# Kernel tuning notes

Hardware: AMD Instinct MI355X
Metric: run time of the kernel (lower is better)

Reference implementation:

```python
import jax, jax.numpy as jnp
import numpy as np

B, N, D, E = 128, 512, 256, 8192  # graphs, nodes/graph, embed_dim, edges/graph
K = int(np.ceil(0.8 * N))         # TopKPooling ratio=0.8 -> k per graph


def setup_inputs() -> dict:
    key = jax.random.key(0)
    ks = jax.random.split(key, 16)
    Ntot = B * N
    x = jax.random.normal(ks[0], (Ntot, 4), jnp.float32)
    offs = (jnp.arange(B, dtype=jnp.int32) * N)[:, None]
    src = (jax.random.randint(ks[1], (B, E), 0, N, jnp.int32) + offs).reshape(-1)
    dst = (jax.random.randint(ks[2], (B, E), 0, N, jnp.int32) + offs).reshape(-1)
    s = 0.05
    w = lambda k, shape: jax.random.normal(k, shape, jnp.float32) * s
    return {
        'x': x, 'src': src, 'dst': dst,
        'Wr1': w(ks[3], (4, D)), 'Ws1': w(ks[4], (4, D)), 'b1': jnp.zeros((D,), jnp.float32),
        'Wr2': w(ks[5], (D, D)), 'Ws2': w(ks[6], (D, D)), 'b2': jnp.zeros((D,), jnp.float32),
        'Wr3': w(ks[7], (D, D)), 'Ws3': w(ks[8], (D, D)), 'b3': jnp.zeros((D,), jnp.float32),
        'p_attn': w(ks[9], (D,)),
        'W1': w(ks[10], (2 * D, D)), 'c1': jnp.zeros((D,), jnp.float32),
        'W2': w(ks[11], (D, D // 2)), 'c2': jnp.zeros((D // 2,), jnp.float32),
        'W3': w(ks[12], (D // 2, 1)), 'c3': jnp.zeros((1,), jnp.float32),
    }


def _graph_conv(x, src, dst, Wr, Ws, b):
    # PyG GraphConv, aggr='add': out = lin_rel(sum_{j in N(i)} x_j) + lin_root(x_i)
    agg = jax.ops.segment_sum(x[src], dst, num_segments=B * N)
    return agg @ Wr + b + x @ Ws


def _gmp_gap(xb):
    # xb: [B, n, D] -> concat(global max pool, global mean pool): [B, 2D]
    return jnp.concatenate([xb.max(axis=1), xb.mean(axis=1)], axis=1)


def reference(x, src, dst, Wr1, Ws1, b1, Wr2, Ws2, b2, Wr3, Ws3, b3,
              p_attn, W1, c1, W2, c2, W3, c3):
    h = jax.nn.relu(_graph_conv(x, src, dst, Wr1, Ws1, b1))
    x1 = _gmp_gap(h.reshape(B, N, D))
    h = jax.nn.relu(_graph_conv(h, src, dst, Wr2, Ws2, b2))
    x2 = _gmp_gap(h.reshape(B, N, D))
    h = jax.nn.relu(_graph_conv(h, src, dst, Wr3, Ws3, b3))
    # TopKPooling: score = x.p/||p||; keep top-k per graph; scale by tanh(score)
    score = (h @ p_attn) / (jnp.linalg.norm(p_attn) + 1e-16)
    vals, idx = jax.lax.top_k(score.reshape(B, N), K)           # [B, K]
    hb = h.reshape(B, N, D)
    sel = jnp.take_along_axis(hb, idx[:, :, None], axis=1) * jnp.tanh(vals)[:, :, None]
    x3 = _gmp_gap(sel)
    z = x1 + x2 + x3
    z = jax.nn.relu(z @ W1 + c1)
    z = jax.nn.relu(z @ W2 + c2)  # dropout is identity in eval mode
    return jax.nn.sigmoid(z @ W3 + c3)[:, 0]
```

## Files before the change

kernel.cpp:

```cpp
#include <hip/hip_runtime.h>

typedef unsigned short u16;
typedef unsigned int u32;

#define B_GRAPHS 128
#define N_NODES  512
#define D_DIM    256
#define E_EDGES  8192
#define K_TOP    410
#define CSR_STRIDE 12288

typedef __attribute__((ext_vector_type(8))) __bf16 bf16x8;
typedef __attribute__((ext_vector_type(4))) float  f32x4;

__device__ __forceinline__ float bf2f(u16 h) {
  union { u32 u; float f; } c; c.u = ((u32)h) << 16; return c.f;
}
__device__ __forceinline__ float u2f(u32 u) {
  union { u32 u; float f; } c; c.u = u; return c.f;
}
__device__ __forceinline__ u16 f2bf(float f) {
  union { float f; u32 u; } c; c.f = f;
  u32 u = c.u;
  u += 0x7fffu + ((u >> 16) & 1u);
  return (u16)(u >> 16);
}
__device__ __forceinline__ void async_copy16(const void* g, void* l) {
  __builtin_amdgcn_global_load_lds((const __attribute__((address_space(1))) void*)g,
                                   (__attribute__((address_space(3))) void*)l, 16, 0, 0);
}

__global__ void zero_kernel(float* __restrict__ p) {
  *(float4*)&p[(size_t)(blockIdx.x * 256 + threadIdx.x) * 4] = float4{0.f, 0.f, 0.f, 0.f};
}

__global__ void prep_kernel(const float* __restrict__ Wr2, const float* __restrict__ Ws2,
                            const float* __restrict__ Wr3, const float* __restrict__ Ws3,
                            u16* __restrict__ WT) {
  const int mat = blockIdx.y;
  const int n = blockIdx.x;
  const int k = threadIdx.x;
  const float* W = (mat == 0) ? Wr2 : (mat == 1) ? Ws2 : (mat == 2) ? Wr3 : Ws3;
  WT[((size_t)mat << 16) + ((size_t)n << 8) + k] = f2bf(W[(size_t)k * 256 + n]);
}

__global__ __launch_bounds__(256) void csr_kernel(const int* __restrict__ src,
                                                  const int* __restrict__ dst,
                                                  u16* __restrict__ csr_col,
                                                  u32* __restrict__ csr_off) {
  __shared__ u32 cnt[512];
  __shared__ u32 scan[512];
  __shared__ u32 poff[513];
  const int g = blockIdx.x, t = threadIdx.x;
  const int base = g * N_NODES, ebase = g * E_EDGES;
  for (int i = t; i < 512; i += 256) cnt[i] = 0;
  __syncthreads();
  for (int e = t; e < E_EDGES; e += 256)
    atomicAdd(&cnt[dst[ebase + e] - base], 1u);
  __syncthreads();
  for (int i = t; i < 512; i += 256) scan[i] = (cnt[i] + 7u) & ~7u;
  __syncthreads();
  #pragma unroll 1
  for (int d = 1; d < 512; d <<= 1) {
    const u32 v0 = (t >= d) ? scan[t - d] : 0u;
    const u32 v1 = scan[t + 256 - d];
    __syncthreads();
    if (t >= d) scan[t] += v0;
    scan[t + 256] += v1;
    __syncthreads();
  }
  if (t == 0) poff[0] = 0;
  for (int i = t; i < 512; i += 256) poff[i + 1] = scan[i];
  __syncthreads();
  for (int i = t; i < 513; i += 256) csr_off[(size_t)g * 513 + i] = poff[i];
  for (int i = t; i < 512; i += 256) {
    const u32 s = poff[i] + cnt[i], e2 = poff[i + 1];
    for (u32 k = s; k < e2; ++k) csr_col[(size_t)g * CSR_STRIDE + k] = 16384;
  }
  __syncthreads();
  for (int i = t; i < 512; i += 256) cnt[i] = poff[i];
  __syncthreads();
  for (int e = t; e < E_EDGES; e += 256) {
    const int d = dst[ebase + e] - base;
    const int s = src[ebase + e] - base;
    const u32 pos = atomicAdd(&cnt[d], 1u);
    csr_col[(size_t)g * CSR_STRIDE + pos] = (u16)(s << 5);
  }
}

__global__ __launch_bounds__(512) void build_a_kernel(const u16* __restrict__ csr_col,
                                                      const u32* __restrict__ csr_off,
                                                      u32* __restrict__ A4) {
  __shared__ unsigned char cnt8[128 * 512];
  __shared__ __align__(16) u16 colsL[CSR_STRIDE];
  const int c = blockIdx.x, g = blockIdx.y;
  const int t = threadIdx.x;
  #pragma unroll
  for (int i = 0; i < 8; ++i)
    ((uint4*)cnt8)[i * 512 + t] = uint4{0u, 0u, 0u, 0u};
  for (int i = t; i < CSR_STRIDE / 2; i += 512)
    ((u32*)colsL)[i] = ((const u32*)(csr_col + (size_t)g * CSR_STRIDE))[i];
  __syncthreads();
  if (t < 128) {
    const int row = c * 128 + t;
    const u32 s0 = csr_off[(size_t)g * 513 + row];
    const u32 s1 = csr_off[(size_t)g * 513 + row + 1];
    for (u32 k = s0; k < s1; ++k) {
      const int col = colsL[k] >> 5;
      if (col < 512) cnt8[t * 512 + col]++;
    }
  }
  __syncthreads();
  u32* outp = A4 + (size_t)(g * 4 + c) * 8192;
  for (int i = t; i < 8192; i += 512) {
    const int row = i >> 6, wd = i & 63;
    const u32 lo = ((const u32*)cnt8)[i * 2];
    const u32 hi = ((const u32*)cnt8)[i * 2 + 1];
    const u32 a = lo | (lo >> 4);
    const u32 b = hi | (hi >> 4);
    const u32 word = (a & 0xffu) | ((a >> 8) & 0xff00u) | ((b << 16) & 0xff0000u)
                   | ((b << 8) & 0xff000000u);
    const int wm2 = row >> 6, mi = (row >> 4) & 3, r16v = row & 15;
    const int stv = wd >> 2, gqv = wd & 3;
    outp[wm2 * 4096 + stv * 256 + mi * 64 + gqv * 16 + r16v] = word;
  }
}

__global__ __launch_bounds__(256) void conv1_kernel(const float* __restrict__ x,
                             const u16* __restrict__ csr_col, const u32* __restrict__ csr_off,
                             const float* __restrict__ Wr1, const float* __restrict__ Ws1,
                             const float* __restrict__ b1,
                             u16* __restrict__ H1, float* __restrict__ X1) {
  __shared__ float xs[513 * 4];
  __shared__ float aggs[N_NODES * 5];
  __shared__ __align__(16) u16 cols[CSR_STRIDE];
  __shared__ u32 offs[513];
  const int c = blockIdx.x;
  const int g = blockIdx.y;
  const int base = g * N_NODES;
  const int t = threadIdx.x;

  for (int i = t; i < N_NODES; i += 256)
    *(float4*)&xs[i * 4] = *(const float4*)&x[(size_t)(base + i) * 4];
  if (t < 4) xs[512 * 4 + t] = 0.f;
  for (int i = t; i < CSR_STRIDE / 2; i += 256)
    ((u32*)cols)[i] = ((const u32*)(csr_col + (size_t)g * CSR_STRIDE))[i];
  for (int i = t; i < 513; i += 256) offs[i] = csr_off[(size_t)g * 513 + i];
  __syncthreads();

  #pragma unroll
  for (int nn = 0; nn < 2; ++nn) {
    const int i = t * 2 + nn;
    const u32 s0 = offs[i];
    const int nb = (int)((offs[i + 1] - s0) >> 3);
    float a0 = 0.f, a1 = 0.f, a2 = 0.f, a3 = 0.f;
    for (int b = 0; b < nb; ++b) {
      const uint4 cw = *(const uint4*)&cols[s0 + (u32)b * 8];
      const u32 ww[4] = {cw.x, cw.y, cw.z, cw.w};
      #pragma unroll
      for (int q = 0; q < 4; ++q) {
        const int ca = (int)((ww[q] & 0xffffu) >> 5);
        const int cb = (int)(ww[q] >> 21);
        const float4 va = *(const float4*)&xs[ca * 4];
        const float4 vb = *(const float4*)&xs[cb * 4];
        a0 += va.x + vb.x; a1 += va.y + vb.y;
        a2 += va.z + vb.z; a3 += va.w + vb.w;
      }
    }
    aggs[i * 5 + 0] = a0; aggs[i * 5 + 1] = a1;
    aggs[i * 5 + 2] = a2; aggs[i * 5 + 3] = a3;
  }
  __syncthreads();

  float wr[4], wsv[4];
  #pragma unroll
  for (int k = 0; k < 4; ++k) { wr[k] = Wr1[k * 256 + t]; wsv[k] = Ws1[k * 256 + t]; }
  const float bb = b1[t];
  float mx = 0.f, sm = 0.f;
  const int nlo = c * 256;
  for (int n = nlo; n < nlo + 256; ++n) {
    float acc = bb;
    #pragma unroll
    for (int k = 0; k < 4; ++k) acc += aggs[n * 5 + k] * wr[k] + xs[n * 4 + k] * wsv[k];
    acc = fmaxf(acc, 0.f);
    H1[(size_t)(base + n) * D_DIM + t] = f2bf(acc);
    mx = fmaxf(mx, acc);
    sm += acc;
  }
  atomicMax((int*)&X1[(size_t)g * 512 + t], __float_as_int(mx));
  atomicAdd(&X1[(size_t)g * 512 + 256 + t], sm);
}

__device__ __forceinline__ bf16x8 decode_a4(u32 a) {
  union { u32 w[4]; bf16x8 v; } r;
  #pragma unroll
  for (int p = 0; p < 4; ++p) {
    const float f0 = (float)((a >> (8 * p)) & 15u);
    const float f1 = (float)((a >> (8 * p + 4)) & 15u);
    r.w[p] = (__float_as_uint(f0) >> 16) | (__float_as_uint(f1) & 0xffff0000u);
  }
  return r.v;
}

__global__ __launch_bounds__(512) void agg_mfma_kernel(const u16* __restrict__ H,
                                                       const u32* __restrict__ A4,
                                                       u16* __restrict__ AGG) {
  __shared__ __align__(16) u16 HtL[8192];
  const int bid = blockIdx.x;
  const int lb = (bid >> 3) + (bid & 7) * 64;
  const int g = lb >> 2, cdst = lb & 3;
  const int gbase = g * 512;
  const int dstbase = cdst * 128;
  const int t = threadIdx.x;
  const int w = t >> 6, lane = t & 63;
  const int wm = w >> 2, wf = w & 3;
  const int r16 = lane & 15, gq = lane >> 4;

  const int oct = t >> 4, sp = t & 15;
  const u16* Hg = H + (size_t)gbase * 256;
  const size_t goff = (size_t)(2 * sp) * 256 + oct * 8;
  const int so = (sp >> 2) ^ (oct & 3);
  int wb[4];
  #pragma unroll
  for (int k = 0; k < 4; ++k) wb[k] = oct * 512 + (sp & 3) * 4 + ((so ^ k) << 4);

  const int subE = gq ^ ((r16 >> 1) & 3) ^ (r16 >> 3);
  const int rbE = wf * 4096 + r16 * 64 + (subE << 4);
  const int rbO = wf * 4096 + r16 * 64 + ((subE ^ 2) << 4);

  const u32* ApB = A4 + (size_t)(g * 4 + cdst) * 8192 + wm * 4096 + lane;

  f32x4 acc[4][4];
  const f32x4 zero = {0.f, 0.f, 0.f, 0.f};
  #pragma unroll
  for (int mi = 0; mi < 4; ++mi)
    #pragma unroll
    for (int ft = 0; ft < 4; ++ft) acc[mi][ft] = zero;

  uint4 rA = *(const uint4*)&Hg[goff];
  uint4 rB = *(const uint4*)&Hg[goff + 256];
  u32 aw[4], awn[4];
  #pragma unroll
  for (int mi = 0; mi < 4; ++mi) aw[mi] = ApB[mi * 64];
  uint4 rAn, rBn;

  #pragma unroll 1
  for (int st = 0; st < 16; ++st) {
    if (st < 15) {
      const size_t noff = goff + (size_t)(st + 1) * 32 * 256;
      rAn = *(const uint4*)&Hg[noff];
      rBn = *(const uint4*)&Hg[noff + 256];
      #pragma unroll
      for (int mi = 0; mi < 4; ++mi) awn[mi] = ApB[(st + 1) * 256 + mi * 64];
    }

    {
      const u32 wa[4] = {rA.x, rA.y, rA.z, rA.w};
      const u32 wbv[4] = {rB.x, rB.y, rB.z, rB.w};
      #pragma unroll
      for (int p = 0; p < 4; ++p) {
        const u32 ve = (wa[p] & 0xffffu) | (wbv[p] << 16);
        const u32 vo = (wa[p] >> 16) | (wbv[p] & 0xffff0000u);
        *(u32*)((char*)HtL + wb[p] + (2 * p) * 64) = ve;
        *(u32*)((char*)HtL + wb[p] + (2 * p + 1) * 64) = vo;
      }
    }
    asm volatile("s_waitcnt lgkmcnt(0)" ::: "memory");
    __builtin_amdgcn_s_barrier();

    bf16x8 aF[4];
    #pragma unroll
    for (int mi = 0; mi < 4; ++mi) aF[mi] = decode_a4(aw[mi]);
    bf16x8 bF[4];
    bF[0] = *(const bf16x8*)((const char*)HtL + rbE);
    bF[1] = *(const bf16x8*)((const char*)HtL + rbO + 1024);
    bF[2] = *(const bf16x8*)((const char*)HtL + rbE + 2048);
    bF[3] = *(const bf16x8*)((const char*)HtL + rbO + 3072);
    #pragma unroll
    for (int mi = 0; mi < 4; ++mi)
      #pragma unroll
      for (int ft = 0; ft < 4; ++ft)
        acc[mi][ft] = __builtin_amdgcn_mfma_f32_16x16x32_bf16(aF[mi], bF[ft],
                                                              acc[mi][ft], 0, 0, 0);
    __builtin_amdgcn_s_barrier();
    rA = rAn; rB = rBn;
    #pragma unroll
    for (int mi = 0; mi < 4; ++mi) aw[mi] = awn[mi];
  }

  #pragma unroll
  for (int mi = 0; mi < 4; ++mi) {
    const size_t rowb = (size_t)(gbase + dstbase + wm * 64 + mi * 16 + gq * 4) * 256;
    #pragma unroll
    for (int ft = 0; ft < 4; ++ft) {
      const int col = wf * 64 + ft * 16 + r16;
      #pragma unroll
      for (int r = 0; r < 4; ++r)
        AGG[rowb + (size_t)r * 256 + col] = f2bf(acc[mi][ft][r]);
    }
  }
}

__global__ __launch_bounds__(512) void gemm_kernel(const u16* __restrict__ Amat,
                                                   const u16* __restrict__ Hmat,
                                                   const u16* __restrict__ WrT,
                                                   const u16* __restrict__ WsT,
                                                   const float* __restrict__ bias,
                                                   u16* __restrict__ Hout,
                                                   float* __restrict__ x2pool,
                                                   float* __restrict__ score,
                                                   const float* __restrict__ pvec) {
  __shared__ __align__(16) u16 At[2][256 * 32];
  __shared__ __align__(16) u16 Bt[2][128 * 32];
  const int m0 = blockIdx.x * 256;
  const int n0 = blockIdx.y * 128;
  const int t = threadIdx.x;
  const int wid = t >> 6, lane = t & 63;
  const int wm = wid >> 1, wn = wid & 1;
  const int r16 = lane & 15, q0 = lane >> 4;

  f32x4 acc[4][4];
  const f32x4 zero = {0.f, 0.f, 0.f, 0.f};
  #pragma unroll
  for (int i = 0; i < 4; ++i)
    #pragma unroll
    for (int jj = 0; jj < 4; ++jj) acc[i][jj] = zero;

  const int srow_off = lane >> 2;
  const int sq = lane & 3;

  auto stage = [&](int s) {
    const int buf = s & 1;
    const int ph = s >> 3;
    const int kk = (s & 7) * 32;
    const u16* Ain = ph ? Hmat : Amat;
    const u16* Win = ph ? WsT : WrT;
    #pragma unroll
    for (int j = 0; j < 3; ++j) {
      const int chk = wid * 3 + j;
      if (chk < 16) {
        const int r = chk * 16 + srow_off;
        const int qsrc = sq ^ ((r >> 1) & 3);
        async_copy16(&Ain[(size_t)(m0 + r) * 256 + kk + qsrc * 8], &At[buf][chk * 512]);
      } else {
        const int ch = chk - 16;
        const int r = ch * 16 + srow_off;
        const int qsrc = sq ^ ((r >> 1) & 3);
        async_copy16(&Win[(size_t)(n0 + r) * 256 + kk + qsrc * 8], &Bt[buf][ch * 512]);
      }
    }
  };

  stage(0);
  #pragma unroll 1
  for (int s = 0; s < 16; ++s) {
    if (s < 15) {
      stage(s + 1);
      asm volatile("s_waitcnt vmcnt(3)" ::: "memory");
    } else {
      asm volatile("s_waitcnt vmcnt(0)" ::: "memory");
    }
    __builtin_amdgcn_s_barrier();
    const int buf = s & 1;
    bf16x8 aF[4], bF[4];
    #pragma unroll
    for (int mi = 0; mi < 4; ++mi) {
      const int arow = wm * 64 + mi * 16 + r16;
      const int qs = q0 ^ ((arow >> 1) & 3);
      aF[mi] = *(const bf16x8*)&At[buf][arow * 32 + qs * 8];
    }
    #pragma unroll
    for (int ni = 0; ni < 4; ++ni) {
      const int brow = wn * 64 + ni * 16 + r16;
      const int qs = q0 ^ ((brow >> 1) & 3);
      bF[ni] = *(const bf16x8*)&Bt[buf][brow * 32 + qs * 8];
    }
    #pragma unroll
    for (int mi = 0; mi < 4; ++mi)
      #pragma unroll
      for (int ni = 0; ni < 4; ++ni)
        acc[mi][ni] = __builtin_amdgcn_mfma_f32_16x16x32_bf16(aF[mi], bF[ni],
                                                              acc[mi][ni], 0, 0, 0);
    __builtin_amdgcn_s_barrier();
  }

  const bool do_x2 = (x2pool != nullptr);
  const bool do_sc = (score != nullptr);
  float colmax[4], colsum[4], pv[4], rpart[4][4];
  #pragma unroll
  for (int ni = 0; ni < 4; ++ni) { colmax[ni] = 0.f; colsum[ni] = 0.f; pv[ni] = 0.f; }
  #pragma unroll
  for (int mi = 0; mi < 4; ++mi)
    #pragma unroll
    for (int r = 0; r < 4; ++r) rpart[mi][r] = 0.f;
  if (do_sc) {
    #pragma unroll
    for (int ni = 0; ni < 4; ++ni) pv[ni] = pvec[n0 + wn * 64 + ni * 16 + r16];
  }

  #pragma unroll
  for (int mi = 0; mi < 4; ++mi) {
    const int growb = m0 + wm * 64 + mi * 16 + q0 * 4;
    #pragma unroll
    for (int ni = 0; ni < 4; ++ni) {
      const int gcol = n0 + wn * 64 + ni * 16 + r16;
      const float bv = bias[gcol];
      #pragma unroll
      for (int r = 0; r < 4; ++r) {
        float v = acc[mi][ni][r] + bv;
        v = fmaxf(v, 0.f);
        Hout[(size_t)(growb + r) * 256 + gcol] = f2bf(v);
        colmax[ni] = fmaxf(colmax[ni], v);
        colsum[ni] += v;
        rpart[mi][r] += v * pv[ni];
      }
    }
  }

  const int gg = m0 >> 9;
  if (do_x2) {
    #pragma unroll
    for (int ni = 0; ni < 4; ++ni) {
      const int gcol = n0 + wn * 64 + ni * 16 + r16;
      float cm = colmax[ni], cs = colsum[ni];
      cm = fmaxf(cm, __shfl_xor(cm, 16));
      cm = fmaxf(cm, __shfl_xor(cm, 32));
      cs += __shfl_xor(cs, 16);
      cs += __shfl_xor(cs, 32);
      if (q0 == 0) {
        atomicMax((int*)&x2pool[(size_t)gg * 512 + gcol], __float_as_int(cm));
        atomicAdd(&x2pool[(size_t)gg * 512 + 256 + gcol], cs);
      }
    }
  }
  if (do_sc) {
    #pragma unroll
    for (int mi = 0; mi < 4; ++mi) {
      const int growb = m0 + wm * 64 + mi * 16 + q0 * 4;
      #pragma unroll
      for (int r = 0; r < 4; ++r) {
        float sp = rpart[mi][r];
        sp += __shfl_xor(sp, 1);
        sp += __shfl_xor(sp, 2);
        sp += __shfl_xor(sp, 4);
        sp += __shfl_xor(sp, 8);
        if (r16 == 0) atomicAdd(&score[growb + r], sp);
      }
    }
  }
}

__global__ __launch_bounds__(256) void sort_kernel(const float* __restrict__ score,
                                                   const float* __restrict__ p,
                                                   u16* __restrict__ top_idx,
                                                   float* __restrict__ top_scale) {
  __shared__ float sval[N_NODES];
  __shared__ int sidx[N_NODES];
  __shared__ float wsum[4];
  const int g = blockIdx.x, t = threadIdx.x;

  float pvt = p[t];
  float sq2 = pvt * pvt;
  #pragma unroll
  for (int off = 32; off > 0; off >>= 1) sq2 += __shfl_down(sq2, off);
  if ((t & 63) == 0) wsum[t >> 6] = sq2;
  __syncthreads();
  const float inv_pn = 1.f / (sqrtf(wsum[0] + wsum[1] + wsum[2] + wsum[3]) + 1e-16f);

  for (int n = t; n < N_NODES; n += 256) {
    sval[n] = score[(size_t)g * 512 + n] * inv_pn;
    sidx[n] = n;
  }
  __syncthreads();

  for (int k = 2; k <= N_NODES; k <<= 1) {
    for (int jj = k >> 1; jj > 0; jj >>= 1) {
      const int i = ((t & ~(jj - 1)) << 1) | (t & (jj - 1));
      const int ix = i | jj;
      const bool dirDesc = ((i & k) == 0);
      const float vi = sval[i], vx = sval[ix];
      const int ii = sidx[i], ij = sidx[ix];
      const bool iAfter = (vi < vx) || (vi == vx && ii > ij);
      if (dirDesc ? iAfter : !iAfter) {
        sval[i] = vx; sval[ix] = vi;
        sidx[i] = ij; sidx[ix] = ii;
      }
      __syncthreads();
    }
  }

  for (int s = t; s < K_TOP; s += 256) {
    top_idx[(size_t)g * 416 + s] = (u16)sidx[s];
    top_scale[(size_t)g * 416 + s] = tanhf(sval[s]);
  }
}

__global__ __launch_bounds__(256) void x3_pool_kernel(const u16* __restrict__ H3,
                                                      const u16* __restrict__ top_idx,
                                                      const float* __restrict__ top_scale,
                                                      float* __restrict__ X3) {
  __shared__ u16 sidxL[416];
  __shared__ float ssclL[416];
  __shared__ float redm[32 * 65];
  __shared__ float reds[32 * 65];
  const int c = blockIdx.x;
  const int g = blockIdx.y;
  const int t = threadIdx.x;
  const int fl = t & 7, rg = t >> 3;

  for (int s = t; s < K_TOP; s += 256) {
    sidxL[s] = top_idx[(size_t)g * 416 + s];
    ssclL[s] = top_scale[(size_t)g * 416 + s];
  }
  __syncthreads();

  float mx[8], sm[8];
  #pragma unroll
  for (int j = 0; j < 8; ++j) { mx[j] = -1e30f; sm[j] = 0.f; }
  const size_t rowbase = (size_t)g * 512;
  for (int s = rg; s < K_TOP; s += 32) {
    const int row = sidxL[s];
    const float sc = ssclL[s];
    const uint4 d = *(const uint4*)&H3[(rowbase + row) * 256 + c * 64 + fl * 8];
    const u32 wv[4] = {d.x, d.y, d.z, d.w};
    #pragma unroll
    for (int q = 0; q < 4; ++q) {
      const float v0 = u2f(wv[q] << 16) * sc;
      const float v1 = u2f(wv[q] & 0xffff0000u) * sc;
      mx[q * 2] = fmaxf(mx[q * 2], v0); sm[q * 2] += v0;
      mx[q * 2 + 1] = fmaxf(mx[q * 2 + 1], v1); sm[q * 2 + 1] += v1;
    }
  }
  #pragma unroll
  for (int j = 0; j < 8; ++j) {
    redm[rg * 65 + fl * 8 + j] = mx[j];
    reds[rg * 65 + fl * 8 + j] = sm[j];
  }
  __syncthreads();
  for (int st = 16; st >= 1; st >>= 1) {
    if (rg < st) {
      #pragma unroll
      for (int j = 0; j < 8; ++j) {
        const int a = rg * 65 + fl * 8 + j, b = (rg + st) * 65 + fl * 8 + j;
        redm[a] = fmaxf(redm[a], redm[b]);
        reds[a] += reds[b];
      }
    }
    __syncthreads();
  }
  if (rg == 0) {
    #pragma unroll
    for (int j = 0; j < 8; ++j) {
      X3[(size_t)g * 512 + c * 64 + fl * 8 + j] = redm[fl * 8 + j];
      X3[(size_t)g * 512 + 256 + c * 64 + fl * 8 + j] = reds[fl * 8 + j] * (1.f / (float)K_TOP);
    }
  }
}

__global__ void mlp_kernel(const float* __restrict__ X1, const float* __restrict__ X2,
                           const float* __restrict__ X3,
                           const float* __restrict__ W1, const float* __restrict__ c1,
                           const float* __restrict__ W2, const float* __restrict__ c2,
                           const float* __restrict__ W3, const float* __restrict__ c3,
                           float* __restrict__ out) {
  __shared__ float zs[512];
  __shared__ float z1[256];
  __shared__ float z2[128];
  const int g = blockIdx.x, t = threadIdx.x;
  for (int k = t; k < 512; k += 256) {
    const float x1v = X1[(size_t)g * 512 + k];
    const float x2v = X2[(size_t)g * 512 + k];
    const float x3v = X3[(size_t)g * 512 + k];
    zs[k] = (k < 256) ? (x1v + x2v + x3v)
                      : (x1v * (1.f / 512.f) + x2v * (1.f / 512.f) + x3v);
  }
  __syncthreads();
  {
    float acc = c1[t];
    for (int k = 0; k < 512; ++k) acc += zs[k] * W1[(size_t)k * 256 + t];
    z1[t] = fmaxf(acc, 0.f);
  }
  __syncthreads();
  if (t < 128) {
    float acc = c2[t];
    for (int d = 0; d < 256; ++d) acc += z1[d] * W2[(size_t)d * 128 + t];
    z2[t] = fmaxf(acc, 0.f);
  }
  __syncthreads();
  if (t == 0) {
    float acc = c3[0];
    for (int e = 0; e < 128; ++e) acc += z2[e] * W3[e];
    out[g] = 1.f / (1.f + expf(-acc));
  }
}

extern "C" void kernel_launch(void* const* d_in, const int* in_sizes, int n_in,
                              void* d_out, int out_size, void* d_ws, size_t ws_size,
                              hipStream_t stream) {
  (void)in_sizes; (void)n_in; (void)out_size; (void)ws_size;
  const float* x   = (const float*)d_in[0];
  const int* src   = (const int*)d_in[1];
  const int* dstp  = (const int*)d_in[2];
  const float* Wr1 = (const float*)d_in[3];
  const float* Ws1 = (const float*)d_in[4];
  const float* b1  = (const float*)d_in[5];
  const float* Wr2 = (const float*)d_in[6];
  const float* Ws2 = (const float*)d_in[7];
  const float* b2  = (const float*)d_in[8];
  const float* Wr3 = (const float*)d_in[9];
  const float* Ws3 = (const float*)d_in[10];
  const float* b3  = (const float*)d_in[11];
  const float* pat = (const float*)d_in[12];
  const float* W1  = (const float*)d_in[13];
  const float* c1  = (const float*)d_in[14];
  const float* W2  = (const float*)d_in[15];
  const float* c2  = (const float*)d_in[16];
  const float* W3  = (const float*)d_in[17];
  const float* c3  = (const float*)d_in[18];
  float* out = (float*)d_out;

  char* ws = (char*)d_ws;
  u16* hA  = (u16*)(ws);
  u16* hB  = (u16*)(ws + 33554432);
  u16* AGG = (u16*)(ws + 67108864);
  u16* WT  = (u16*)(ws + 100663296);
  float* x1 = (float*)(ws + 101187584);
  float* x2 = (float*)(ws + 101449728);
  float* x3 = (float*)(ws + 101711872);
  u16* csr_col = (u16*)(ws + 101974016);
  u32* csr_off = (u32*)(ws + 105119744);
  u32* A4u     = (u32*)(ws + 105383936);
  float* score     = (float*)(ws + 101974016);
  u16* top_idx     = (u16*)(ws + 101974016 + 262144);
  float* top_scale = (float*)(ws + 101974016 + 372736);

  prep_kernel<<<dim3(256, 4), dim3(256), 0, stream>>>(Wr2, Ws2, Wr3, Ws3, WT);
  csr_kernel<<<dim3(128), dim3(256), 0, stream>>>(src, dstp, csr_col, csr_off);
  zero_kernel<<<dim3(128), dim3(256), 0, stream>>>(x1);
  build_a_kernel<<<dim3(4, 128), dim3(512), 0, stream>>>(csr_col, csr_off, A4u);
  conv1_kernel<<<dim3(2, 128), dim3(256), 0, stream>>>(x, csr_col, csr_off, Wr1, Ws1, b1, hA, x1);

  agg_mfma_kernel<<<dim3(512), dim3(512), 0, stream>>>(hA, A4u, AGG);
  gemm_kernel<<<dim3(256, 2), dim3(512), 0, stream>>>(AGG, hA, WT, WT + 65536, b2, hB,
                                                      x2, nullptr, nullptr);

  agg_mfma_kernel<<<dim3(512), dim3(512), 0, stream>>>(hB, A4u, AGG);
  zero_kernel<<<dim3(64), dim3(256), 0, stream>>>(score);
  gemm_kernel<<<dim3(256, 2), dim3(512), 0, stream>>>(AGG, hB, WT + 131072, WT + 196608, b3, hA,
                                                      nullptr, score, pat);

  sort_kernel<<<dim3(128), dim3(256), 0, stream>>>(score, pat, top_idx, top_scale);
  x3_pool_kernel<<<dim3(4, 128), dim3(256), 0, stream>>>(hA, top_idx, top_scale, x3);
  mlp_kernel<<<dim3(128), dim3(256), 0, stream>>>(x1, x2, x3, W1, c1, W2, c2, W3, c3, out);
}
```

Before: 264.4 us.

## Fuse adjacency aggregation MFMA with GraphConv GEMM and keep AGG tile in LDS

Merges the aggregation kernel and the dense GraphConv GEMM into one kernel per 128-row destination tile. The aggregated tile stays in a 64KB swizzled LDS buffer instead of going through a global AGG array, and each block computes all 256 output columns, streaming weight chunks through a small LDS buffer. This removes the AGG write and re-read and one launch per layer. In exchange, LDS use per block rises, which may lower occupancy. The weight loads are no longer double-buffered (wait vmcnt(0) each step), and the root-term A operands are read straight from global memory without staging.

```diff
diff --git a/kernel.cpp b/kernel.cpp
--- a/kernel.cpp
+++ b/kernel.cpp
@@ -202,10 +202,17 @@
   return r.v;
 }
 
-__global__ __launch_bounds__(512) void agg_mfma_kernel(const u16* __restrict__ H,
-                                                       const u32* __restrict__ A4,
-                                                       u16* __restrict__ AGG) {
-  __shared__ __align__(16) u16 HtL[8192];
+__global__ __launch_bounds__(512) void fused_layer_kernel(const u16* __restrict__ H,
+                                                          const u32* __restrict__ A4,
+                                                          const u16* __restrict__ WrT,
+                                                          const u16* __restrict__ WsT,
+                                                          const float* __restrict__ bias,
+                                                          u16* __restrict__ Hout,
+                                                          float* __restrict__ x2pool,
+                                                          float* __restrict__ score,
+                                                          const float* __restrict__ pvec) {
+  __shared__ __align__(16) u16 T[128 * 256];
+  __shared__ __align__(16) u16 SB[8192];
   const int bid = blockIdx.x;
   const int lb = (bid >> 3) + (bid & 7) * 64;
   const int g = lb >> 2, cdst = lb & 3;
@@ -216,171 +223,146 @@
   const int wm = w >> 2, wf = w & 3;
   const int r16 = lane & 15, gq = lane >> 4;
 
-  const int oct = t >> 4, sp = t & 15;
-  const u16* Hg = H + (size_t)gbase * 256;
-  const size_t goff = (size_t)(2 * sp) * 256 + oct * 8;
-  const int so = (sp >> 2) ^ (oct & 3);
-  int wb[4];
-  #pragma unroll
-  for (int k = 0; k < 4; ++k) wb[k] = oct * 512 + (sp & 3) * 4 + ((so ^ k) << 4);
-
-  const int subE = gq ^ ((r16 >> 1) & 3) ^ (r16 >> 3);
-  const int rbE = wf * 4096 + r16 * 64 + (subE << 4);
-  const int rbO = wf * 4096 + r16 * 64 + ((subE ^ 2) << 4);
-
-  const u32* ApB = A4 + (size_t)(g * 4 + cdst) * 8192 + wm * 4096 + lane;
-
-  f32x4 acc[4][4];
-  const f32x4 zero = {0.f, 0.f, 0.f, 0.f};
+  {
+    const int oct = t >> 4, sp = t & 15;
+    const u16* Hg = H + (size_t)gbase * 256;
+    const size_t goff = (size_t)(2 * sp) * 256 + oct * 8;
+    const int so = (sp >> 2) ^ (oct & 3);
+    int wb[4];
+    #pragma unroll
+    for (int k = 0; k < 4; ++k) wb[k] = oct * 512 + (sp & 3) * 4 + ((so ^ k) << 4);
+
+    const int subE = gq ^ ((r16 >> 1) & 3) ^ (r16 >> 3);
+    const int rbE = wf * 4096 + r16 * 64 + (subE << 4);
+    const int rbO = wf * 4096 + r16 * 64 + ((subE ^ 2) << 4);
+
+    const u32* ApB = A4 + (size_t)(g * 4 + cdst) * 8192 + wm * 4096 + lane;
+
+    f32x4 acc[4][4];
+    const f32x4 zero = {0.f, 0.f, 0.f, 0.f};
+    #pragma unroll
+    for (int mi = 0; mi < 4; ++mi)
+      #pragma unroll
+      for (int ft = 0; ft < 4; ++ft) acc[mi][ft] = zero;
+
+    uint4 rA = *(const uint4*)&Hg[goff];
+    uint4 rB = *(const uint4*)&Hg[goff + 256];
+    u32 aw[4], awn[4];
+    #pragma unroll
+    for (int mi = 0; mi < 4; ++mi) aw[mi] = ApB[mi * 64];
+    uint4 rAn, rBn;
+
+    #pragma unroll 1
+    for (int st = 0; st < 16; ++st) {
+      if (st < 15) {
+        const size_t noff = goff + (size_t)(st + 1) * 32 * 256;
+        rAn = *(const uint4*)&Hg[noff];
+        rBn = *(const uint4*)&Hg[noff + 256];
+        #pragma unroll
+        for (int mi = 0; mi < 4; ++mi) awn[mi] = ApB[(st + 1) * 256 + mi * 64];
+      }
+      {
+        const u32 wa[4] = {rA.x, rA.y, rA.z, rA.w};
+        const u32 wbv[4] = {rB.x, rB.y, rB.z, rB.w};
+        #pragma unroll
+        for (int p = 0; p < 4; ++p) {
+          const u32 ve = (wa[p] & 0xffffu) | (wbv[p] << 16);
+          const u32 vo = (wa[p] >> 16) | (wbv[p] & 0xffff0000u);
+          *(u32*)((char*)SB + wb[p] + (2 * p) * 64) = ve;
+          *(u32*)((char*)SB + wb[p] + (2 * p + 1) * 64) = vo;
+        }
+      }
+      asm volatile("s_waitcnt lgkmcnt(0)" ::: "memory");
+      __builtin_amdgcn_s_barrier();
+
+      bf16x8 aF[4];
+      #pragma unroll
+      for (int mi = 0; mi < 4; ++mi) aF[mi] = decode_a4(aw[mi]);
+      bf16x8 bF[4];
+      bF[0] = *(const bf16x8*)((const char*)SB + rbE);
+      bF[1] = *(const bf16x8*)((const char*)SB + rbO + 1024);
+      bF[2] = *(const bf16x8*)((const char*)SB + rbE + 2048);
+      bF[3] = *(const bf16x8*)((const char*)SB + rbO + 3072);
+      #pragma unroll
+      for (int mi = 0; mi < 4; ++mi)
+        #pragma unroll
+        for (int ft = 0; ft < 4; ++ft)
+          acc[mi][ft] = __builtin_amdgcn_mfma_f32_16x16x32_bf16(aF[mi], bF[ft],
+                                                                acc[mi][ft], 0, 0, 0);
+      __builtin_amdgcn_s_barrier();
+      rA = rAn; rB = rBn;
+      #pragma unroll
+      for (int mi = 0; mi < 4; ++mi) aw[mi] = awn[mi];
+    }
+
+    #pragma unroll
+    for (int mi = 0; mi < 4; ++mi) {
+      #pragma unroll
+      for (int ft = 0; ft < 4; ++ft) {
+        const int col = wf * 64 + ft * 16 + r16;
+        const int q = (col >> 3) & 3, cb = col & ~31, b = col & 7;
+        #pragma unroll
+        for (int r = 0; r < 4; ++r) {
+          const int row = wm * 64 + mi * 16 + gq * 4 + r;
+          const int scol = cb | (((q ^ ((row >> 1) & 3)) << 3) | b);
+          T[row * 256 + scol] = f2bf(acc[mi][ft][r]);
+        }
+      }
+    }
+  }
+  __syncthreads();
+
+  const int wc = w & 3;
+  f32x4 acc2[4][4];
+  const f32x4 zero2 = {0.f, 0.f, 0.f, 0.f};
   #pragma unroll
   for (int mi = 0; mi < 4; ++mi)
     #pragma unroll
-    for (int ft = 0; ft < 4; ++ft) acc[mi][ft] = zero;
-
-  uint4 rA = *(const uint4*)&Hg[goff];
-  uint4 rB = *(const uint4*)&Hg[goff + 256];
-  u32 aw[4], awn[4];
-  #pragma unroll
-  for (int mi = 0; mi < 4; ++mi) aw[mi] = ApB[mi * 64];
-  uint4 rAn, rBn;
-
-  #pragma unroll 1
-  for (int st = 0; st < 16; ++st) {
-    if (st < 15) {
-      const size_t noff = goff + (size_t)(st + 1) * 32 * 256;
-      rAn = *(const uint4*)&Hg[noff];
-      rBn = *(const uint4*)&Hg[noff + 256];
-      #pragma unroll
-      for (int mi = 0; mi < 4; ++mi) awn[mi] = ApB[(st + 1) * 256 + mi * 64];
-    }
-
-    {
-      const u32 wa[4] = {rA.x, rA.y, rA.z, rA.w};
-      const u32 wbv[4] = {rB.x, rB.y, rB.z, rB.w};
-      #pragma unroll
-      for (int p = 0; p < 4; ++p) {
-        const u32 ve = (wa[p] & 0xffffu) | (wbv[p] << 16);
-        const u32 vo = (wa[p] >> 16) | (wbv[p] & 0xffff0000u);
-        *(u32*)((char*)HtL + wb[p] + (2 * p) * 64) = ve;
-        *(u32*)((char*)HtL + wb[p] + (2 * p + 1) * 64) = vo;
-      }
-    }
-    asm volatile("s_waitcnt lgkmcnt(0)" ::: "memory");
-    __builtin_amdgcn_s_barrier();
-
-    bf16x8 aF[4];
-    #pragma unroll
-    for (int mi = 0; mi < 4; ++mi) aF[mi] = decode_a4(aw[mi]);
-    bf16x8 bF[4];
-    bF[0] = *(const bf16x8*)((const char*)HtL + rbE);
-    bF[1] = *(const bf16x8*)((const char*)HtL + rbO + 1024);
-    bF[2] = *(const bf16x8*)((const char*)HtL + rbE + 2048);
-    bF[3] = *(const bf16x8*)((const char*)HtL + rbO + 3072);
-    #pragma unroll
-    for (int mi = 0; mi < 4; ++mi)
-      #pragma unroll
-      for (int ft = 0; ft < 4; ++ft)
-        acc[mi][ft] = __builtin_amdgcn_mfma_f32_16x16x32_bf16(aF[mi], bF[ft],
-                                                              acc[mi][ft], 0, 0, 0);
-    __builtin_amdgcn_s_barrier();
-    rA = rAn; rB = rBn;
-    #pragma unroll
-    for (int mi = 0; mi < 4; ++mi) aw[mi] = awn[mi];
-  }
-
-  #pragma unroll
-  for (int mi = 0; mi < 4; ++mi) {
-    const size_t rowb = (size_t)(gbase + dstbase + wm * 64 + mi * 16 + gq * 4) * 256;
-    #pragma unroll
-    for (int ft = 0; ft < 4; ++ft) {
-      const int col = wf * 64 + ft * 16 + r16;
-      #pragma unroll
-      for (int r = 0; r < 4; ++r)
-        AGG[rowb + (size_t)r * 256 + col] = f2bf(acc[mi][ft][r]);
-    }
-  }
-}
-
-__global__ __launch_bounds__(512) void gemm_kernel(const u16* __restrict__ Amat,
-                                                   const u16* __restrict__ Hmat,
-                                                   const u16* __restrict__ WrT,
-                                                   const u16* __restrict__ WsT,
-                                                   const float* __restrict__ bias,
-                                                   u16* __restrict__ Hout,
-                                                   float* __restrict__ x2pool,
-                                                   float* __restrict__ score,
-                                                   const float* __restrict__ pvec) {
-  __shared__ __align__(16) u16 At[2][256 * 32];
-  __shared__ __align__(16) u16 Bt[2][128 * 32];
-  const int m0 = blockIdx.x * 256;
-  const int n0 = blockIdx.y * 128;
-  const int t = threadIdx.x;
-  const int wid = t >> 6, lane = t & 63;
-  const int wm = wid >> 1, wn = wid & 1;
-  const int r16 = lane & 15, q0 = lane >> 4;
-
-  f32x4 acc[4][4];
-  const f32x4 zero = {0.f, 0.f, 0.f, 0.f};
-  #pragma unroll
-  for (int i = 0; i < 4; ++i)
-    #pragma unroll
-    for (int jj = 0; jj < 4; ++jj) acc[i][jj] = zero;
-
-  const int srow_off = lane >> 2;
-  const int sq = lane & 3;
-
-  auto stage = [&](int s) {
-    const int buf = s & 1;
-    const int ph = s >> 3;
-    const int kk = (s & 7) * 32;
-    const u16* Ain = ph ? Hmat : Amat;
-    const u16* Win = ph ? WsT : WrT;
-    #pragma unroll
-    for (int j = 0; j < 3; ++j) {
-      const int chk = wid * 3 + j;
-      if (chk < 16) {
-        const int r = chk * 16 + srow_off;
-        const int qsrc = sq ^ ((r >> 1) & 3);
-        async_copy16(&Ain[(size_t)(m0 + r) * 256 + kk + qsrc * 8], &At[buf][chk * 512]);
-      } else {
-        const int ch = chk - 16;
-        const int r = ch * 16 + srow_off;
-        const int qsrc = sq ^ ((r >> 1) & 3);
-        async_copy16(&Win[(size_t)(n0 + r) * 256 + kk + qsrc * 8], &Bt[buf][ch * 512]);
-      }
-    }
-  };
-
-  stage(0);
+    for (int nc = 0; nc < 4; ++nc) acc2[mi][nc] = zero2;
+
+  const u16* Hd = H + (size_t)(gbase + dstbase) * 256;
+
   #pragma unroll 1
   for (int s = 0; s < 16; ++s) {
-    if (s < 15) {
-      stage(s + 1);
-      asm volatile("s_waitcnt vmcnt(3)" ::: "memory");
+    const u16* Win = (s < 8) ? WrT : WsT;
+    const int kk = (s & 7) * 32;
+    #pragma unroll
+    for (int j = 0; j < 2; ++j) {
+      const int chk = w * 2 + j;
+      const int n = chk * 16 + (lane >> 2);
+      const int qsrc = (lane & 3) ^ ((n >> 1) & 3);
+      async_copy16(&Win[(size_t)n * 256 + kk + qsrc * 8], &SB[chk * 512]);
+    }
+    asm volatile("s_waitcnt vmcnt(0)" ::: "memory");
+    __builtin_amdgcn_s_barrier();
+
+    bf16x8 aF[4], bF[4];
+    if (s < 8) {
+      #pragma unroll
+      for (int mi = 0; mi < 4; ++mi) {
+        const int arow = wm * 64 + mi * 16 + r16;
+        const int qs = gq ^ ((arow >> 1) & 3);
+        aF[mi] = *(const bf16x8*)&T[arow * 256 + kk + qs * 8];
+      }
     } else {
-      asm volatile("s_waitcnt vmcnt(0)" ::: "memory");
-    }
-    __builtin_amdgcn_s_barrier();
-    const int buf = s & 1;
-    bf16x8 aF[4], bF[4];
-    #pragma unroll
-    for (int mi = 0; mi < 4; ++mi) {
-      const int arow = wm * 64 + mi * 16 + r16;
-      const int qs = q0 ^ ((arow >> 1) & 3);
-      aF[mi] = *(const bf16x8*)&At[buf][arow * 32 + qs * 8];
-    }
-    #pragma unroll
-    for (int ni = 0; ni < 4; ++ni) {
-      const int brow = wn * 64 + ni * 16 + r16;
-      const int qs = q0 ^ ((brow >> 1) & 3);
-      bF[ni] = *(const bf16x8*)&Bt[buf][brow * 32 + qs * 8];
+      #pragma unroll
+      for (int mi = 0; mi < 4; ++mi) {
+        const int arow = wm * 64 + mi * 16 + r16;
+        aF[mi] = *(const bf16x8*)&Hd[(size_t)arow * 256 + kk + gq * 8];
+      }
+    }
+    #pragma unroll
+    for (int nc = 0; nc < 4; ++nc) {
+      const int brow = wc * 64 + nc * 16 + r16;
+      const int qs = gq ^ ((brow >> 1) & 3);
+      bF[nc] = *(const bf16x8*)&SB[brow * 32 + qs * 8];
     }
     #pragma unroll
     for (int mi = 0; mi < 4; ++mi)
       #pragma unroll
-      for (int ni = 0; ni < 4; ++ni)
-        acc[mi][ni] = __builtin_amdgcn_mfma_f32_16x16x32_bf16(aF[mi], bF[ni],
-                                                              acc[mi][ni], 0, 0, 0);
+      for (int nc = 0; nc < 4; ++nc)
+        acc2[mi][nc] = __builtin_amdgcn_mfma_f32_16x16x32_bf16(aF[mi], bF[nc],
+                                                               acc2[mi][nc], 0, 0, 0);
     __builtin_amdgcn_s_barrier();
   }
 
@@ -388,55 +370,54 @@
   const bool do_sc = (score != nullptr);
   float colmax[4], colsum[4], pv[4], rpart[4][4];
   #pragma unroll
-  for (int ni = 0; ni < 4; ++ni) { colmax[ni] = 0.f; colsum[ni] = 0.f; pv[ni] = 0.f; }
+  for (int nc = 0; nc < 4; ++nc) { colmax[nc] = 0.f; colsum[nc] = 0.f; pv[nc] = 0.f; }
   #pragma unroll
   for (int mi = 0; mi < 4; ++mi)
     #pragma unroll
     for (int r = 0; r < 4; ++r) rpart[mi][r] = 0.f;
   if (do_sc) {
     #pragma unroll
-    for (int ni = 0; ni < 4; ++ni) pv[ni] = pvec[n0 + wn * 64 + ni * 16 + r16];
+    for (int nc = 0; nc < 4; ++nc) pv[nc] = pvec[wc * 64 + nc * 16 + r16];
   }
 
   #pragma unroll
   for (int mi = 0; mi < 4; ++mi) {
-    const int growb = m0 + wm * 64 + mi * 16 + q0 * 4;
-    #pragma unroll
-    for (int ni = 0; ni < 4; ++ni) {
-      const int gcol = n0 + wn * 64 + ni * 16 + r16;
+    const int growb = gbase + dstbase + wm * 64 + mi * 16 + gq * 4;
+    #pragma unroll
+    for (int nc = 0; nc < 4; ++nc) {
+      const int gcol = wc * 64 + nc * 16 + r16;
       const float bv = bias[gcol];
       #pragma unroll
       for (int r = 0; r < 4; ++r) {
-        float v = acc[mi][ni][r] + bv;
+        float v = acc2[mi][nc][r] + bv;
         v = fmaxf(v, 0.f);
         Hout[(size_t)(growb + r) * 256 + gcol] = f2bf(v);
-        colmax[ni] = fmaxf(colmax[ni], v);
-        colsum[ni] += v;
-        rpart[mi][r] += v * pv[ni];
-      }
-    }
-  }
-
-  const int gg = m0 >> 9;
+        colmax[nc] = fmaxf(colmax[nc], v);
+        colsum[nc] += v;
+        rpart[mi][r] += v * pv[nc];
+      }
+    }
+  }
+
   if (do_x2) {
     #pragma unroll
-    for (int ni = 0; ni < 4; ++ni) {
-      const int gcol = n0 + wn * 64 + ni * 16 + r16;
-      float cm = colmax[ni], cs = colsum[ni];
+    for (int nc = 0; nc < 4; ++nc) {
+      const int gcol = wc * 64 + nc * 16 + r16;
+      float cm = colmax[nc], cs = colsum[nc];
       cm = fmaxf(cm, __shfl_xor(cm, 16));
       cm = fmaxf(cm, __shfl_xor(cm, 32));
       cs += __shfl_xor(cs, 16);
       cs += __shfl_xor(cs, 32);
-      if (q0 == 0) {
-        atomicMax((int*)&x2pool[(size_t)gg * 512 + gcol], __float_as_int(cm));
-        atomicAdd(&x2pool[(size_t)gg * 512 + 256 + gcol], cs);
+      if (gq == 0) {
+        atomicMax((int*)&x2pool[(size_t)g * 512 + gcol], __float_as_int(cm));
+        atomicAdd(&x2pool[(size_t)g * 512 + 256 + gcol], cs);
       }
     }
   }
   if (do_sc) {
     #pragma unroll
     for (int mi = 0; mi < 4; ++mi) {
-      const int growb = m0 + wm * 64 + mi * 16 + q0 * 4;
+      const int growb = gbase + dstbase + wm * 64 + mi * 16 + gq * 4;
       #pragma unroll
       for (int r = 0; r < 4; ++r) {
         float sp = rpart[mi][r];
@@ -622,7 +603,6 @@
   char* ws = (char*)d_ws;
   u16* hA  = (u16*)(ws);
   u16* hB  = (u16*)(ws + 33554432);
-  u16* AGG = (u16*)(ws + 67108864);
   u16* WT  = (u16*)(ws + 100663296);
   float* x1 = (float*)(ws + 101187584);
   float* x2 = (float*)(ws + 101449728);
@@ -640,14 +620,12 @@
   build_a_kernel<<<dim3(4, 128), dim3(512), 0, stream>>>(csr_col, csr_off, A4u);
   conv1_kernel<<<dim3(2, 128), dim3(256), 0, stream>>>(x, csr_col, csr_off, Wr1, Ws1, b1, hA, x1);
 
-  agg_mfma_kernel<<<dim3(512), dim3(512), 0, stream>>>(hA, A4u, AGG);
-  gemm_kernel<<<dim3(256, 2), dim3(512), 0, stream>>>(AGG, hA, WT, WT + 65536, b2, hB,
-                                                      x2, nullptr, nullptr);
-
-  agg_mfma_kernel<<<dim3(512), dim3(512), 0, stream>>>(hB, A4u, AGG);
+  fused_layer_kernel<<<dim3(512), dim3(512), 0, stream>>>(hA, A4u, WT, WT + 65536, b2, hB,
+                                                          x2, nullptr, nullptr);
+
   zero_kernel<<<dim3(64), dim3(256), 0, stream>>>(score);
-  gemm_kernel<<<dim3(256, 2), dim3(512), 0, stream>>>(AGG, hB, WT + 131072, WT + 196608, b3, hA,
-                                                      nullptr, score, pat);
+  fused_layer_kernel<<<dim3(512), dim3(512), 0, stream>>>(hB, A4u, WT + 131072, WT + 196608,
+                                                          b3, hA, nullptr, score, pat);
 
   sort_kernel<<<dim3(128), dim3(256), 0, stream>>>(score, pat, top_idx, top_scale);
   x3_pool_kernel<<<dim3(4, 128), dim3(256), 0, stream>>>(hA, top_idx, top_scale, x3);
```

Result: slower. 318.6 us (+20.5%).
